# Performance work log

Hardware: AMD Instinct MI355X
Metric: run time of the kernel (lower is better)

The kernel has to match this reference:

```python
import jax, jax.numpy as jnp
import numpy as np

EMBED = 1024
HEADS = 16
HEAD_DIM = EMBED // HEADS


def setup_inputs() -> dict:
    key = jax.random.key(0)
    k1, k2, k3, k4, k5 = jax.random.split(key, 5)
    B, S = 4, 2048
    scale = 1.0 / np.sqrt(EMBED)
    return {
        "query_features": jax.random.normal(k1, (B, S, EMBED), dtype=jnp.float32),
        "W_qkv": jax.random.normal(k2, (EMBED, 3 * EMBED), dtype=jnp.float32) * scale,
        "b_qkv": jnp.zeros((3 * EMBED,), dtype=jnp.float32),
        "W_out": jax.random.normal(k3, (EMBED, EMBED), dtype=jnp.float32) * scale,
        "b_out": jnp.zeros((EMBED,), dtype=jnp.float32),
    }


def reference(query_features, W_qkv, b_qkv, W_out, b_out):
    B, S, E = query_features.shape
    qkv = jnp.einsum("bse,ef->bsf", query_features, W_qkv) + b_qkv  # [B,S,3E]
    q, k, v = jnp.split(qkv, 3, axis=-1)
    # split heads: [B,H,S,D]
    def heads(x):
        return x.reshape(B, S, HEADS, HEAD_DIM).transpose(0, 2, 1, 3)
    q, k, v = heads(q), heads(k), heads(v)
    scale = 1.0 / np.sqrt(HEAD_DIM)
    scores = jnp.einsum("bhqd,bhkd->bhqk", q, k) * scale
    attn = jax.nn.softmax(scores, axis=-1)
    out = jnp.einsum("bhqk,bhkd->bhqd", attn, v)  # [B,H,S,D]
    out = out.transpose(0, 2, 1, 3).reshape(B, S, E)
    return jnp.einsum("bse,ef->bsf", out, W_out) + b_out
```

## Files before the change

kernel.cpp:

```cpp
#include <hip/hip_runtime.h>
#include <hip/hip_bf16.h>
#include <stdint.h>
#include <stddef.h>

using short8 = __attribute__((ext_vector_type(8))) short;
using short4v = __attribute__((ext_vector_type(4))) short;
using f32x4  = __attribute__((ext_vector_type(4))) float;
typedef __hip_bfloat16 bf16_t;

__device__ __forceinline__ void glds16(const void* g, const void* l) {
  __builtin_amdgcn_global_load_lds(
      (const __attribute__((address_space(1))) void*)g,
      (__attribute__((address_space(3))) void*)l, 16, 0, 0);
}
__device__ __forceinline__ short bfbits(float x) {
  bf16_t h = __float2bfloat16(x);
  return __builtin_bit_cast(short, h);
}

__global__ void dtype_probe(const unsigned short* __restrict__ w, int* flag) {
  int bad = 0;
  for (int i = threadIdx.x; i < 4096; i += 256) {
    float f = __uint_as_float((unsigned)w[i] << 16);
    if (!(fabsf(f) <= 1e10f)) bad = 1;
  }
  if (bad) atomicOr(flag, 1);
}

__global__ __launch_bounds__(256)
void transpose_w(const void* __restrict__ Wv, bf16_t* __restrict__ Wt, int R,
                 int C, const int* __restrict__ flag) {
  __shared__ float tile[32][33];
  const int tx = threadIdx.x, ty = threadIdx.y;
  const int n0 = blockIdx.x * 32, k0 = blockIdx.y * 32;
  const int isf = *flag;
#pragma unroll
  for (int j = 0; j < 4; ++j) {
    const int k = k0 + ty + j * 8;
    tile[ty + j * 8][tx] =
        isf ? ((const float*)Wv)[(size_t)k * C + n0 + tx]
            : __bfloat162float(((const bf16_t*)Wv)[(size_t)k * C + n0 + tx]);
  }
  __syncthreads();
#pragma unroll
  for (int j = 0; j < 4; ++j) {
    const int n = n0 + ty + j * 8;
    Wt[(size_t)n * R + k0 + tx] = __float2bfloat16(tile[tx][ty + j * 8]);
  }
}

__global__ __launch_bounds__(256)
void convert_x(const void* __restrict__ Xv, bf16_t* __restrict__ Xb, int total,
               const int* __restrict__ flag) {
  const int i = (blockIdx.x * 256 + threadIdx.x) * 4;
  if (i >= total) return;
  if (*flag) {
    const float4 v = *(const float4*)((const float*)Xv + i);
    Xb[i + 0] = __float2bfloat16(v.x);
    Xb[i + 1] = __float2bfloat16(v.y);
    Xb[i + 2] = __float2bfloat16(v.z);
    Xb[i + 3] = __float2bfloat16(v.w);
  } else {
    *(uint2*)(Xb + i) = *(const uint2*)((const bf16_t*)Xv + i);
  }
}

template <int MODE>
__global__ __launch_bounds__(256)
void gemm_k(const bf16_t* __restrict__ A, const bf16_t* __restrict__ Bt,
            const void* __restrict__ biasv, void* __restrict__ Cv,
            bf16_t* __restrict__ Qo, bf16_t* __restrict__ Ko,
            bf16_t* __restrict__ Vo, int M, int N, int K,
            const int* __restrict__ flag) {
  __shared__ __align__(16) bf16_t lA[128 * 64];
  __shared__ __align__(16) bf16_t lB[128 * 64];

  const int isf32 = *flag;
  const int tid  = threadIdx.x;
  const int w    = tid >> 6;
  const int lane = tid & 63;
  const int lrow = lane & 15;
  const int quad = lane >> 4;
  const int m0 = blockIdx.x * 128;
  const int n0 = blockIdx.y * 128;
  const int wm = (w >> 1) * 64;
  const int wn = (w & 1) * 64;

  f32x4 acc[4][4];
  for (int i = 0; i < 4; ++i)
    for (int j = 0; j < 4; ++j)
      for (int r = 0; r < 4; ++r) acc[i][j][r] = 0.f;

  for (int kt = 0; kt < K; kt += 64) {
#pragma unroll
    for (int i = 0; i < 4; ++i) {
      const int cbase = i * 256 + w * 64;
      const int c = cbase + lane;
      const int row = c >> 3;
      const int q = (c & 7) ^ (row & 7);
      glds16(A + (size_t)(m0 + row) * K + kt + q * 8,
             (const char*)lA + cbase * 16);
      glds16(Bt + (size_t)(n0 + row) * K + kt + q * 8,
             (const char*)lB + cbase * 16);
    }
    __syncthreads();
#pragma unroll
    for (int ks = 0; ks < 2; ++ks) {
      short8 af[4], bfr[4];
#pragma unroll
      for (int mi = 0; mi < 4; ++mi) {
        const int row = wm + mi * 16 + lrow;
        const int slot = (ks * 4 + quad) ^ (row & 7);
        af[mi] = *(const short8*)((const char*)lA + row * 128 + slot * 16);
      }
#pragma unroll
      for (int ni = 0; ni < 4; ++ni) {
        const int row = wn + ni * 16 + lrow;
        const int slot = (ks * 4 + quad) ^ (row & 7);
        bfr[ni] = *(const short8*)((const char*)lB + row * 128 + slot * 16);
      }
#pragma unroll
      for (int mi = 0; mi < 4; ++mi)
#pragma unroll
        for (int ni = 0; ni < 4; ++ni)
          acc[mi][ni] = __builtin_amdgcn_mfma_f32_16x16x32_bf16(
              af[mi], bfr[ni], acc[mi][ni], 0, 0, 0);
    }
    __syncthreads();
  }

#pragma unroll
  for (int mi = 0; mi < 4; ++mi) {
#pragma unroll
    for (int ni = 0; ni < 4; ++ni) {
      const int col = n0 + wn + ni * 16 + lrow;
      const float bv = isf32 ? ((const float*)biasv)[col]
                             : __bfloat162float(((const bf16_t*)biasv)[col]);
#pragma unroll
      for (int r = 0; r < 4; ++r) {
        const int row = m0 + wm + mi * 16 + quad * 4 + r;
        const float val = acc[mi][ni][r] + bv;
        if (MODE == 0) {
          if (isf32)
            ((float*)Cv)[(size_t)row * N + col] = val;
          else
            ((bf16_t*)Cv)[(size_t)row * N + col] = __float2bfloat16(val);
        } else {
          const bf16_t hv = __float2bfloat16(val);
          const int b = row >> 11, s = row & 2047;
          const int sec = col >> 10, h = (col >> 6) & 15, d = col & 63;
          if (sec == 0)
            Qo[((((size_t)b * 16 + h) * 2048) + s) * 64 + d] = hv;
          else if (sec == 1)
            Ko[((((size_t)b * 16 + h) * 2048) + s) * 64 + d] = hv;
          else
            Vo[((((size_t)b * 16 + h) * 64) + d) * 2048 + s] = hv;
        }
      }
    }
  }
}

__global__ __launch_bounds__(256)
void attn_fwd(const bf16_t* __restrict__ Q, const bf16_t* __restrict__ K,
              const bf16_t* __restrict__ Vt, bf16_t* __restrict__ AO) {
  constexpr float CSC = 0.18033688011112042f;
  constexpr float C0  = 8.0f;
  __shared__ __align__(16) bf16_t lK[64 * 64];
  __shared__ __align__(16) bf16_t lV[64 * 64];

  const int tid  = threadIdx.x;
  const int w    = tid >> 6;
  const int lane = tid & 63;
  const int lrow = lane & 15;
  const int quad = lane >> 4;
  const int id = blockIdx.x;
  const int bh = (id & 7) * 8 + (id >> 7);
  const int q0 = ((id >> 3) & 15) * 128;

  const bf16_t* Qb = Q + (size_t)bh * 2048 * 64;
  const bf16_t* Kb = K + (size_t)bh * 2048 * 64;
  const bf16_t* Vb = Vt + (size_t)bh * 64 * 2048;

  short8 aq[2][2];
#pragma unroll
  for (int qt = 0; qt < 2; ++qt)
#pragma unroll
    for (int ks = 0; ks < 2; ++ks)
      aq[qt][ks] = *(const short8*)(Qb +
          (size_t)(q0 + w * 32 + qt * 16 + lrow) * 64 + ks * 32 + quad * 8);

  f32x4 ot[4][2];
  float lsum[2] = {0.f, 0.f};
#pragma unroll
  for (int dt = 0; dt < 4; ++dt)
    for (int qt = 0; qt < 2; ++qt)
      for (int r = 0; r < 4; ++r) ot[dt][qt][r] = 0.f;

  short8 pk[2], pv[2];
#pragma unroll
  for (int i = 0; i < 2; ++i) {
    const int c = i * 256 + tid, row = c >> 3, ch = c & 7;
    pk[i] = *(const short8*)(Kb + (size_t)row * 64 + ch * 8);
    pv[i] = *(const short8*)(Vb + (size_t)row * 2048 + ch * 8);
  }

  for (int kt = 0; kt < 2048; kt += 64) {
    if (kt) __syncthreads();
#pragma unroll
    for (int i = 0; i < 2; ++i) {
      const int c = i * 256 + tid, row = c >> 3, ch = c & 7;
      const int slot = ch ^ (row & 7);
      *(short8*)((char*)lK + row * 128 + slot * 16) = pk[i];
      *(short8*)((char*)lV + row * 128 + slot * 16) = pv[i];
    }
    __syncthreads();
    if (kt + 64 < 2048) {
#pragma unroll
      for (int i = 0; i < 2; ++i) {
        const int c = i * 256 + tid, row = c >> 3, ch = c & 7;
        pk[i] = *(const short8*)(Kb + (size_t)(kt + 64 + row) * 64 + ch * 8);
        pv[i] = *(const short8*)(Vb + (size_t)row * 2048 + kt + 64 + ch * 8);
      }
    }

    f32x4 sc[4][2];
#pragma unroll
    for (int k4 = 0; k4 < 4; ++k4)
      for (int qt = 0; qt < 2; ++qt)
        for (int r = 0; r < 4; ++r) sc[k4][qt][r] = 0.f;
#pragma unroll
    for (int ks = 0; ks < 2; ++ks) {
      short8 ak[4];
#pragma unroll
      for (int k4 = 0; k4 < 4; ++k4) {
        const int row = k4 * 16 + lrow;
        const int slot = (ks * 4 + quad) ^ (row & 7);
        ak[k4] = *(const short8*)((const char*)lK + row * 128 + slot * 16);
      }
#pragma unroll
      for (int k4 = 0; k4 < 4; ++k4)
#pragma unroll
        for (int qt = 0; qt < 2; ++qt)
          sc[k4][qt] = __builtin_amdgcn_mfma_f32_16x16x32_bf16(
              ak[k4], aq[qt][ks], sc[k4][qt], 0, 0, 0);
    }

#pragma unroll
    for (int kc = 0; kc < 4; ++kc) {
      short4v pf[2];
#pragma unroll
      for (int qt = 0; qt < 2; ++qt) {
#pragma unroll
        for (int r = 0; r < 4; ++r) {
          const float p = __builtin_amdgcn_exp2f(
              __builtin_fmaf(sc[kc][qt][r], CSC, -C0));
          lsum[qt] += p;
          pf[qt][r] = bfbits(p);
        }
      }
#pragma unroll
      for (int dt = 0; dt < 4; ++dt) {
        const int row = dt * 16 + lrow;
        const int ch = kc * 2 + (quad >> 1);
        const int slot = ch ^ (row & 7);
        const short4v vf = *(const short4v*)((const char*)lV + row * 128 +
                                             slot * 16 + (quad & 1) * 8);
#pragma unroll
        for (int qt = 0; qt < 2; ++qt)
          ot[dt][qt] = __builtin_amdgcn_mfma_f32_16x16x16bf16_1k(
              vf, pf[qt], ot[dt][qt], 0, 0, 0);
      }
    }
  }

  const int b = bh >> 4, h = bh & 15;
#pragma unroll
  for (int qt = 0; qt < 2; ++qt) {
    float s = lsum[qt];
    s += __shfl_xor(s, 16, 64);
    s += __shfl_xor(s, 32, 64);
    const float inv = 1.f / s;
    const int srow = q0 + w * 32 + qt * 16 + lrow;
#pragma unroll
    for (int dt = 0; dt < 4; ++dt) {
      uint2 pack;
      short* ps = (short*)&pack;
#pragma unroll
      for (int r = 0; r < 4; ++r) ps[r] = bfbits(ot[dt][qt][r] * inv);
      *(uint2*)(AO + ((size_t)b * 2048 + srow) * 1024 + h * 64 + dt * 16 +
                quad * 4) = pack;
    }
  }
}

extern "C" void kernel_launch(void* const* d_in, const int* in_sizes, int n_in,
                              void* d_out, int out_size, void* d_ws,
                              size_t ws_size, hipStream_t stream) {
  const void* X    = d_in[0];
  const void* Wqkv = d_in[1];
  const void* bqkv = d_in[2];
  const void* Wout = d_in[3];
  const void* bout = d_in[4];

  char* ws = (char*)d_ws;
  bf16_t* WqkvT = (bf16_t*)(ws);
  bf16_t* WoutT = (bf16_t*)(ws + 6291456);
  bf16_t* Qw    = (bf16_t*)(ws + 8388608);
  bf16_t* Kw    = (bf16_t*)(ws + 25165824);
  bf16_t* Vw    = (bf16_t*)(ws + 41943040);
  bf16_t* AOw   = (bf16_t*)(ws + 58720256);
  bf16_t* Xbf   = AOw;
  int*    flag  = (int*)(ws + 75497472);

  hipMemsetAsync(flag, 0, 4, stream);
  dtype_probe<<<1, 256, 0, stream>>>((const unsigned short*)Wqkv, flag);

  transpose_w<<<dim3(96, 32), dim3(32, 8), 0, stream>>>(Wqkv, WqkvT, 1024,
                                                        3072, flag);
  transpose_w<<<dim3(32, 32), dim3(32, 8), 0, stream>>>(Wout, WoutT, 1024,
                                                        1024, flag);
  convert_x<<<8192, 256, 0, stream>>>(X, Xbf, 8388608, flag);

  gemm_k<1><<<dim3(64, 24), 256, 0, stream>>>(Xbf, WqkvT, bqkv, nullptr, Qw,
                                              Kw, Vw, 8192, 3072, 1024, flag);
  attn_fwd<<<1024, 256, 0, stream>>>(Qw, Kw, Vw, AOw);
  gemm_k<0><<<dim3(64, 8), 256, 0, stream>>>(AOw, WoutT, bout, d_out, nullptr,
                                             nullptr, nullptr, 8192, 1024, 1024,
                                             flag);
}
```

Before: 306.7 us.

## Use 16x16x32 MFMA for PV via permuted K rows; vectorize QKV epilogue

The attention kernel now loads K rows in a permuted order so that each lane's score outputs line up with the 8-wide k layout of the 16x16x32 bf16 MFMA. That lets the PV product use the wider instruction with short8 V reads, replacing the 16x16x16 variant. Probabilities are converted to bf16 by truncation and packed with perm, and the row sum uses the truncated values so normalisation stays consistent. The QKV projection epilogue hoists the section and batch index math per block and writes V^T with 4-wide vector stores. The cost is a more intricate LDS swizzle and a slight precision change from truncating instead of rounding.

```diff
diff --git a/kernel.cpp b/kernel.cpp
--- a/kernel.cpp
+++ b/kernel.cpp
@@ -3,9 +3,10 @@
 #include <stdint.h>
 #include <stddef.h>
 
-using short8 = __attribute__((ext_vector_type(8))) short;
+using short8  = __attribute__((ext_vector_type(8))) short;
 using short4v = __attribute__((ext_vector_type(4))) short;
-using f32x4  = __attribute__((ext_vector_type(4))) float;
+using int4v   = __attribute__((ext_vector_type(4))) int;
+using f32x4   = __attribute__((ext_vector_type(4))) float;
 typedef __hip_bfloat16 bf16_t;
 
 __device__ __forceinline__ void glds16(const void* g, const void* l) {
@@ -16,6 +17,14 @@
 __device__ __forceinline__ short bfbits(float x) {
   bf16_t h = __float2bfloat16(x);
   return __builtin_bit_cast(short, h);
+}
+__device__ __forceinline__ int pk2(float lo, float hi) {
+  return __builtin_amdgcn_perm(__builtin_bit_cast(unsigned, hi),
+                               __builtin_bit_cast(unsigned, lo), 0x07060302u);
+}
+__device__ __forceinline__ float truncbf(float x) {
+  return __builtin_bit_cast(float,
+                            __builtin_bit_cast(unsigned, x) & 0xFFFF0000u);
 }
 
 __global__ void dtype_probe(const unsigned short* __restrict__ w, int* flag) {
@@ -129,32 +138,49 @@
     __syncthreads();
   }
 
-#pragma unroll
-  for (int mi = 0; mi < 4; ++mi) {
-#pragma unroll
-    for (int ni = 0; ni < 4; ++ni) {
-      const int col = n0 + wn + ni * 16 + lrow;
-      const float bv = isf32 ? ((const float*)biasv)[col]
-                             : __bfloat162float(((const bf16_t*)biasv)[col]);
-#pragma unroll
-      for (int r = 0; r < 4; ++r) {
-        const int row = m0 + wm + mi * 16 + quad * 4 + r;
-        const float val = acc[mi][ni][r] + bv;
-        if (MODE == 0) {
+  if (MODE == 1) {
+    const int sec = n0 >> 10;
+    const int b = m0 >> 11;
+    const int s0 = (m0 & 2047) + wm + quad * 4;
+#pragma unroll
+    for (int mi = 0; mi < 4; ++mi) {
+#pragma unroll
+      for (int ni = 0; ni < 4; ++ni) {
+        const int col = n0 + wn + ni * 16 + lrow;
+        const float bv = isf32 ? ((const float*)biasv)[col]
+                               : __bfloat162float(((const bf16_t*)biasv)[col]);
+        const int h = (col >> 6) & 15, d = col & 63;
+        const int s = s0 + mi * 16;
+        if (sec == 2) {
+          short4v hv4;
+#pragma unroll
+          for (int r = 0; r < 4; ++r) hv4[r] = bfbits(acc[mi][ni][r] + bv);
+          *(short4v*)(Vo + ((((size_t)b * 16 + h) * 64) + d) * 2048 + s) = hv4;
+        } else {
+          bf16_t* dst = (sec == 0 ? Qo : Ko) +
+                        ((((size_t)b * 16 + h) * 2048) + s) * 64 + d;
+#pragma unroll
+          for (int r = 0; r < 4; ++r)
+            dst[(size_t)r * 64] = __float2bfloat16(acc[mi][ni][r] + bv);
+        }
+      }
+    }
+  } else {
+#pragma unroll
+    for (int mi = 0; mi < 4; ++mi) {
+#pragma unroll
+      for (int ni = 0; ni < 4; ++ni) {
+        const int col = n0 + wn + ni * 16 + lrow;
+        const float bv = isf32 ? ((const float*)biasv)[col]
+                               : __bfloat162float(((const bf16_t*)biasv)[col]);
+#pragma unroll
+        for (int r = 0; r < 4; ++r) {
+          const int row = m0 + wm + mi * 16 + quad * 4 + r;
+          const float val = acc[mi][ni][r] + bv;
           if (isf32)
             ((float*)Cv)[(size_t)row * N + col] = val;
           else
             ((bf16_t*)Cv)[(size_t)row * N + col] = __float2bfloat16(val);
-        } else {
-          const bf16_t hv = __float2bfloat16(val);
-          const int b = row >> 11, s = row & 2047;
-          const int sec = col >> 10, h = (col >> 6) & 15, d = col & 63;
-          if (sec == 0)
-            Qo[((((size_t)b * 16 + h) * 2048) + s) * 64 + d] = hv;
-          else if (sec == 1)
-            Ko[((((size_t)b * 16 + h) * 2048) + s) * 64 + d] = hv;
-          else
-            Vo[((((size_t)b * 16 + h) * 64) + d) * 2048 + s] = hv;
         }
       }
     }
@@ -182,6 +208,9 @@
   const bf16_t* Kb = K + (size_t)bh * 2048 * 64;
   const bf16_t* Vb = Vt + (size_t)bh * 64 * 2048;
 
+  const int rbase = (lrow >> 2) * 8 + (lrow & 3);
+  const int fkl   = 2 * (lrow >> 2) + (lrow & 1);
+
   short8 aq[2][2];
 #pragma unroll
   for (int qt = 0; qt < 2; ++qt)
@@ -210,9 +239,9 @@
 #pragma unroll
     for (int i = 0; i < 2; ++i) {
       const int c = i * 256 + tid, row = c >> 3, ch = c & 7;
-      const int slot = ch ^ (row & 7);
-      *(short8*)((char*)lK + row * 128 + slot * 16) = pk[i];
-      *(short8*)((char*)lV + row * 128 + slot * 16) = pv[i];
+      const int fk = 2 * ((row >> 3) & 3) + (row & 1);
+      *(short8*)((char*)lK + row * 128 + (ch ^ fk) * 16) = pk[i];
+      *(short8*)((char*)lV + row * 128 + (ch ^ (row & 7)) * 16) = pv[i];
     }
     __syncthreads();
     if (kt + 64 < 2048) {
@@ -224,52 +253,64 @@
       }
     }
 
-    f32x4 sc[4][2];
-#pragma unroll
-    for (int k4 = 0; k4 < 4; ++k4)
-      for (int qt = 0; qt < 2; ++qt)
-        for (int r = 0; r < 4; ++r) sc[k4][qt][r] = 0.f;
+    f32x4 sc[2][2][2];
+#pragma unroll
+    for (int g = 0; g < 2; ++g)
+      for (int T = 0; T < 2; ++T)
+        for (int qt = 0; qt < 2; ++qt)
+          for (int r = 0; r < 4; ++r) sc[g][T][qt][r] = 0.f;
 #pragma unroll
     for (int ks = 0; ks < 2; ++ks) {
-      short8 ak[4];
-#pragma unroll
-      for (int k4 = 0; k4 < 4; ++k4) {
-        const int row = k4 * 16 + lrow;
-        const int slot = (ks * 4 + quad) ^ (row & 7);
-        ak[k4] = *(const short8*)((const char*)lK + row * 128 + slot * 16);
-      }
-#pragma unroll
-      for (int k4 = 0; k4 < 4; ++k4)
-#pragma unroll
-        for (int qt = 0; qt < 2; ++qt)
-          sc[k4][qt] = __builtin_amdgcn_mfma_f32_16x16x32_bf16(
-              ak[k4], aq[qt][ks], sc[k4][qt], 0, 0, 0);
-    }
-
-#pragma unroll
-    for (int kc = 0; kc < 4; ++kc) {
-      short4v pf[2];
+      short8 ak[2][2];
+#pragma unroll
+      for (int g = 0; g < 2; ++g)
+#pragma unroll
+        for (int T = 0; T < 2; ++T) {
+          const int row = g * 32 + T * 4 + rbase;
+          const int slot = (ks * 4 + quad) ^ fkl;
+          ak[g][T] = *(const short8*)((const char*)lK + row * 128 + slot * 16);
+        }
+#pragma unroll
+      for (int g = 0; g < 2; ++g)
+#pragma unroll
+        for (int T = 0; T < 2; ++T)
+#pragma unroll
+          for (int qt = 0; qt < 2; ++qt)
+            sc[g][T][qt] = __builtin_amdgcn_mfma_f32_16x16x32_bf16(
+                ak[g][T], aq[qt][ks], sc[g][T][qt], 0, 0, 0);
+    }
+
+#pragma unroll
+    for (int g = 0; g < 2; ++g) {
+      short8 pb[2];
 #pragma unroll
       for (int qt = 0; qt < 2; ++qt) {
-#pragma unroll
-        for (int r = 0; r < 4; ++r) {
-          const float p = __builtin_amdgcn_exp2f(
-              __builtin_fmaf(sc[kc][qt][r], CSC, -C0));
-          lsum[qt] += p;
-          pf[qt][r] = bfbits(p);
-        }
+        float p[8];
+#pragma unroll
+        for (int T = 0; T < 2; ++T)
+#pragma unroll
+          for (int r = 0; r < 4; ++r) {
+            float e = __builtin_amdgcn_exp2f(
+                __builtin_fmaf(sc[g][T][qt][r], CSC, -C0));
+            e = truncbf(e);
+            p[T * 4 + r] = e;
+            lsum[qt] += e;
+          }
+        int4v pi = {pk2(p[0], p[1]), pk2(p[2], p[3]), pk2(p[4], p[5]),
+                    pk2(p[6], p[7])};
+        pb[qt] = __builtin_bit_cast(short8, pi);
       }
 #pragma unroll
       for (int dt = 0; dt < 4; ++dt) {
         const int row = dt * 16 + lrow;
-        const int ch = kc * 2 + (quad >> 1);
+        const int ch = g * 4 + quad;
         const int slot = ch ^ (row & 7);
-        const short4v vf = *(const short4v*)((const char*)lV + row * 128 +
-                                             slot * 16 + (quad & 1) * 8);
+        const short8 vf =
+            *(const short8*)((const char*)lV + row * 128 + slot * 16);
 #pragma unroll
         for (int qt = 0; qt < 2; ++qt)
-          ot[dt][qt] = __builtin_amdgcn_mfma_f32_16x16x16bf16_1k(
-              vf, pf[qt], ot[dt][qt], 0, 0, 0);
+          ot[dt][qt] = __builtin_amdgcn_mfma_f32_16x16x32_bf16(
+              vf, pb[qt], ot[dt][qt], 0, 0, 0);
       }
     }
   }
```

Result: faster. 287.0 us (-6.4%).
